# Optimization experiments

Measured on AMD Instinct MI355X. Metric: run time of the kernel, lower is better.

The kernel has to match this reference:

```python
import jax, jax.numpy as jnp
import numpy as np

L, D, H, HD, FF, V, NH, S = 5, 1024, 8, 128, 4096, 2048, 15, 2
EPS = 1e-6
THETA = 10000.0


def rms_norm(x, w):
    x32 = x.astype(jnp.float32)
    y = x32 * jax.lax.rsqrt(jnp.mean(x32 * x32, axis=-1, keepdims=True) + EPS)
    return (y * w.astype(jnp.float32)).astype(x.dtype)


def rotate_half(x):
    x1, x2 = x[..., : HD // 2], x[..., HD // 2:]
    return jnp.concatenate((-x2, x1), axis=-1)


def setup_inputs() -> dict:
    key = jax.random.key(0)
    ks = jax.random.split(key, 20)
    s = 0.02
    inp = {
        "past_hidden": jax.random.normal(ks[0], (1, 1, D), jnp.float32),
        "cb0_token": jax.random.randint(ks[1], (1, 1), 0, V, jnp.int32),
        "codec_emb": jax.random.normal(ks[2], (V, D), jnp.float32) * s,
        "Wq": jax.random.normal(ks[3], (L, D, H * HD), jnp.float32) * s,
        "Wk": jax.random.normal(ks[4], (L, D, H * HD), jnp.float32) * s,
        "Wv": jax.random.normal(ks[5], (L, D, H * HD), jnp.float32) * s,
        "Wo": jax.random.normal(ks[6], (L, H * HD, D), jnp.float32) * s,
        "q_norm_w": jnp.ones((L, HD), jnp.float32),
        "k_norm_w": jnp.ones((L, HD), jnp.float32),
        "ln1_w": jnp.ones((L, D), jnp.float32),
        "ln2_w": jnp.ones((L, D), jnp.float32),
        "Wgate": jax.random.normal(ks[7], (L, D, FF), jnp.float32) * s,
        "Wup": jax.random.normal(ks[8], (L, D, FF), jnp.float32) * s,
        "Wdown": jax.random.normal(ks[9], (L, FF, D), jnp.float32) * s,
        "final_norm_w": jnp.ones((D,), jnp.float32),
        "lm_heads": jax.random.normal(ks[10], (NH, D, V), jnp.float32) * s,
    }
    return inp


def reference(past_hidden, codec_emb, Wq, Wk, Wv, Wo, q_norm_w, k_norm_w,
              ln1_w, ln2_w, Wgate, Wup, Wdown, final_norm_w, lm_heads,
              cb0_token):
    # Embed CB0 token and build 2-token prefill sequence [1, 2, D].
    cb0_embed = codec_emb[cb0_token]            # [1, 1, D]
    h = jnp.concatenate([past_hidden, cb0_embed], axis=1)

    # Rotary cos/sin for positions [0, 1]: [1, 1, S, HD].
    pos = jnp.arange(S, dtype=jnp.float32)
    inv_freq = 1.0 / (THETA ** (jnp.arange(0, HD, 2, dtype=jnp.float32) / HD))
    freqs = pos[:, None] * inv_freq[None, :]    # [S, HD/2]
    emb = jnp.concatenate([freqs, freqs], axis=-1)
    cos = jnp.cos(emb)[None, None]
    sin = jnp.sin(emb)[None, None]

    causal_mask = jnp.array([[0.0, -1e9], [0.0, 0.0]], jnp.float32)
    scale = 1.0 / np.sqrt(HD)

    def layer_step(h, p):
        wq, wk, wv, wo, qn, kn, l1, l2, wg, wu, wd = p
        res = h
        x = rms_norm(h, l1)                     # [1, S, D]
        q = (x @ wq).reshape(1, S, H, HD)
        k = (x @ wk).reshape(1, S, H, HD)
        v = (x @ wv).reshape(1, S, H, HD)
        q = rms_norm(q, qn)                     # per-head qk-norm
        k = rms_norm(k, kn)
        q = q.transpose(0, 2, 1, 3)             # [1, H, S, HD]
        k = k.transpose(0, 2, 1, 3)
        v = v.transpose(0, 2, 1, 3)
        q = q * cos + rotate_half(q) * sin
        k = k * cos + rotate_half(k) * sin
        attn = jnp.einsum('bhqd,bhkd->bhqk', q, k) * scale + causal_mask
        w = jax.nn.softmax(attn.astype(jnp.float32), axis=-1).astype(q.dtype)
        o = jnp.einsum('bhqk,bhkd->bhqd', w, v)
        o = o.transpose(0, 2, 1, 3).reshape(1, S, H * HD) @ wo
        h = res + o
        res = h
        x = rms_norm(h, l2)
        mlp = (jax.nn.silu(x @ wg) * (x @ wu)) @ wd
        return res + mlp, (k, v)

    h, (ks_, vs_) = jax.lax.scan(
        layer_step, h,
        (Wq, Wk, Wv, Wo, q_norm_w, k_norm_w, ln1_w, ln2_w, Wgate, Wup, Wdown))

    h = rms_norm(h, final_norm_w)
    last = h[:, -1, :]                          # [1, D]
    all_logits = jnp.einsum('bd,ndv->nbv', last, lm_heads)  # [15, 1, V]
    # Interleave keys/values per layer: [2L, 1, H, S, HD].
    kv_cache = jnp.stack([ks_, vs_], axis=1).reshape(2 * L, 1, H, S, HD)
    return all_logits, kv_cache
```

## Files before the change

kernel.cpp:

```cpp
#include <hip/hip_runtime.h>
#include <math.h>

#define EPS 1e-6f


__device__ __forceinline__ float red32(float v) {
#pragma unroll
    for (int m = 16; m >= 1; m >>= 1) v += __shfl_xor(v, m, 64);
    return v;
}

__global__ void init_kernel(const float* __restrict__ past_hidden,
                            const float* __restrict__ codec_emb,
                            const int* __restrict__ tok,
                            float* __restrict__ ws,
                            float* __restrict__ logits)
{
    size_t idx = (size_t)blockIdx.x * blockDim.x + threadIdx.x;
    size_t stride = (size_t)gridDim.x * blockDim.x;
    for (size_t i = idx; i < 30720; i += stride) ws[2048 + i] = 0.f;
    for (size_t i = idx; i < 81920; i += stride) ws[43008 + i] = 0.f;
    for (size_t i = idx; i < 30720; i += stride) logits[i] = 0.f;
    int t = tok[0];
    for (size_t i = idx; i < 1024; i += stride) {
        ws[i]        = past_hidden[i];
        ws[1024 + i] = codec_emb[(size_t)t * 1024 + i];
    }
}

template <int S, int R>
__global__ __launch_bounds__(256) void gemv_rms(
    const float* __restrict__ hbuf,
    const float* __restrict__ nw,
    const float* __restrict__ W0,
    const float* __restrict__ W1,
    const float* __restrict__ W2,
    size_t w_zstride,
    float* __restrict__ out,
    int out_sstride, int out_zstride, int N)
{
    __shared__ float xs[S * 1024];
    __shared__ float sstot[S * 4];
    const int t = threadIdx.x;
    const int lane = t & 63;
    const int dp = t >> 6;

    const float* W;
    if (W1) W = (blockIdx.z == 0) ? W0 : ((blockIdx.z == 1) ? W1 : W2);
    else    W = W0 + (size_t)blockIdx.z * w_zstride;
    float* outz = out + (size_t)blockIdx.z * out_zstride;

    const int j = blockIdx.x * 256 + lane * 4;
    const int d0 = blockIdx.y * (4 * R) + dp * R;

    float4 wreg[R];
    const float* Wp = W + (size_t)d0 * N + j;
#pragma unroll
    for (int i = 0; i < R; ++i)
        wreg[i] = *reinterpret_cast<const float4*>(Wp + (size_t)i * N);

    float ss[S];
    {
        float4 nw4 = *reinterpret_cast<const float4*>(nw + t * 4);
#pragma unroll
        for (int s = 0; s < S; ++s) {
            float4 xv = *reinterpret_cast<const float4*>(hbuf + s * 1024 + t * 4);
            ss[s] = xv.x * xv.x + xv.y * xv.y + xv.z * xv.z + xv.w * xv.w;
            float4 xw = make_float4(xv.x * nw4.x, xv.y * nw4.y, xv.z * nw4.z, xv.w * nw4.w);
            *reinterpret_cast<float4*>(&xs[s * 1024 + t * 4]) = xw;
        }
    }
    __syncthreads();

    float acc[S][4];
#pragma unroll
    for (int s = 0; s < S; ++s) { acc[s][0] = acc[s][1] = acc[s][2] = acc[s][3] = 0.f; }
#pragma unroll
    for (int i = 0; i < R; ++i) {
        int dd = d0 + i;
#pragma unroll
        for (int s = 0; s < S; ++s) {
            float xv = xs[s * 1024 + dd];
            acc[s][0] += xv * wreg[i].x; acc[s][1] += xv * wreg[i].y;
            acc[s][2] += xv * wreg[i].z; acc[s][3] += xv * wreg[i].w;
        }
    }

#pragma unroll
    for (int s = 0; s < S; ++s) {
        float v = ss[s];
#pragma unroll
        for (int m = 32; m >= 1; m >>= 1) v += __shfl_xor(v, m, 64);
        if (lane == 0) sstot[s * 4 + dp] = v;
    }
    __syncthreads();
    float sc[S];
#pragma unroll
    for (int s = 0; s < S; ++s) {
        float tot = sstot[s * 4 + 0] + sstot[s * 4 + 1] + sstot[s * 4 + 2] + sstot[s * 4 + 3];
        sc[s] = rsqrtf(tot / 1024.f + EPS);
    }

#pragma unroll
    for (int s = 0; s < S; ++s)
#pragma unroll
        for (int c = 0; c < 4; ++c)
            xs[(dp * S + s) * 256 + lane * 4 + c] = acc[s][c] * sc[s];
    __syncthreads();
    for (int o = t; o < S * 256; o += 256) {
        int s = o >> 8;
        int col = o & 255;
        float sum = 0.f;
#pragma unroll
        for (int p = 0; p < 4; ++p) sum += xs[(p * S + s) * 256 + col];
        atomicAdd(outz + (size_t)s * out_sstride + blockIdx.x * 256 + col, sum);
    }
}

__global__ __launch_bounds__(256) void attn_o_kernel(
    const float* __restrict__ qkv,
    const float* __restrict__ qnw,
    const float* __restrict__ knw,
    const float* __restrict__ W,
    float* __restrict__ out,
    float* __restrict__ kvc)
{
    __shared__ float xs[2048];
    const int t = threadIdx.x;
    const int lane = t & 63;
    const int dp = t >> 6;
    const int j = blockIdx.x * 256 + lane * 4;
    const int d0 = blockIdx.y * 16 + dp * 4;

    float4 wreg[4];
    const float* Wp = W + (size_t)d0 * 1024 + j;
#pragma unroll
    for (int i = 0; i < 4; ++i)
        wreg[i] = *reinterpret_cast<const float4*>(Wp + (size_t)i * 1024);

    const int hh = t >> 5;
    const int g = t & 31;
    float q[2][4], k[2][4], v[2][4];
#pragma unroll
    for (int s = 0; s < 2; ++s)
#pragma unroll
        for (int c = 0; c < 4; ++c) {
            int d = g + c * 32;
            q[s][c] = qkv[s * 3072 +        hh * 128 + d];
            k[s][c] = qkv[s * 3072 + 1024 + hh * 128 + d];
            v[s][c] = qkv[s * 3072 + 2048 + hh * 128 + d];
        }
#pragma unroll
    for (int s = 0; s < 2; ++s) {
        float sq = q[s][0]*q[s][0] + q[s][1]*q[s][1] + q[s][2]*q[s][2] + q[s][3]*q[s][3];
        float sk = k[s][0]*k[s][0] + k[s][1]*k[s][1] + k[s][2]*k[s][2] + k[s][3]*k[s][3];
        sq = red32(sq); sk = red32(sk);
        float qsc = rsqrtf(sq / 128.f + EPS);
        float ksc = rsqrtf(sk / 128.f + EPS);
#pragma unroll
        for (int c = 0; c < 4; ++c) {
            q[s][c] *= qsc * qnw[g + c * 32];
            k[s][c] *= ksc * knw[g + c * 32];
        }
    }
    float inv0 = powf(10000.f, -(float)g / 64.f);
    float inv1 = powf(10000.f, -(float)(g + 32) / 64.f);
    float cA = cosf(inv0), sA = sinf(inv0);
    float cB = cosf(inv1), sB = sinf(inv1);
    float q1[4] = { q[1][0]*cA - q[1][2]*sA, q[1][1]*cB - q[1][3]*sB,
                    q[1][2]*cA + q[1][0]*sA, q[1][3]*cB + q[1][1]*sB };
    float k1[4] = { k[1][0]*cA - k[1][2]*sA, k[1][1]*cB - k[1][3]*sB,
                    k[1][2]*cA + k[1][0]*sA, k[1][3]*cB + k[1][1]*sB };

    if (blockIdx.x == 0 && blockIdx.y == 0) {
#pragma unroll
        for (int c = 0; c < 4; ++c) {
            int d = g + c * 32;
            kvc[hh * 256 +       d] = k[0][c];
            kvc[hh * 256 + 128 + d] = k1[c];
            kvc[2048 + hh * 256 +       d] = v[0][c];
            kvc[2048 + hh * 256 + 128 + d] = v[1][c];
        }
    }

    float p00 = red32(q[0][0]*k[0][0] + q[0][1]*k[0][1] + q[0][2]*k[0][2] + q[0][3]*k[0][3]);
    float p01 = red32(q[0][0]*k1[0]   + q[0][1]*k1[1]   + q[0][2]*k1[2]   + q[0][3]*k1[3]);
    float p10 = red32(q1[0]*k[0][0]   + q1[1]*k[0][1]   + q1[2]*k[0][2]   + q1[3]*k[0][3]);
    float p11 = red32(q1[0]*k1[0]     + q1[1]*k1[1]     + q1[2]*k1[2]     + q1[3]*k1[3]);

    const float scale = 0.08838834764831845f;
    float s00 = p00 * scale, s01 = p01 * scale - 1e9f;
    float m0 = fmaxf(s00, s01);
    float e0 = expf(s00 - m0), e1 = expf(s01 - m0);
    float in0 = 1.f / (e0 + e1);
    float w00 = e0 * in0, w01 = e1 * in0;
    float s10 = p10 * scale, s11 = p11 * scale;
    float m1 = fmaxf(s10, s11);
    float f0 = expf(s10 - m1), f1 = expf(s11 - m1);
    float in1 = 1.f / (f0 + f1);
    float w10 = f0 * in1, w11 = f1 * in1;

#pragma unroll
    for (int c = 0; c < 4; ++c) {
        int d = g + c * 32;
        xs[       hh * 128 + d] = w00 * v[0][c] + w01 * v[1][c];
        xs[1024 + hh * 128 + d] = w10 * v[0][c] + w11 * v[1][c];
    }
    __syncthreads();

    float acc[2][4] = {{0.f,0.f,0.f,0.f},{0.f,0.f,0.f,0.f}};
#pragma unroll
    for (int i = 0; i < 4; ++i) {
        int dd = d0 + i;
#pragma unroll
        for (int s = 0; s < 2; ++s) {
            float xv = xs[s * 1024 + dd];
            acc[s][0] += xv * wreg[i].x; acc[s][1] += xv * wreg[i].y;
            acc[s][2] += xv * wreg[i].z; acc[s][3] += xv * wreg[i].w;
        }
    }
    __syncthreads();
#pragma unroll
    for (int s = 0; s < 2; ++s)
#pragma unroll
        for (int c = 0; c < 4; ++c)
            xs[(dp * 2 + s) * 256 + lane * 4 + c] = acc[s][c];
    __syncthreads();
    for (int o = t; o < 512; o += 256) {
        int s = o >> 8, col = o & 255;
        float sum = 0.f;
#pragma unroll
        for (int p = 0; p < 4; ++p) sum += xs[(p * 2 + s) * 256 + col];
        atomicAdd(out + (size_t)s * 1024 + blockIdx.x * 256 + col, sum);
    }
}

__global__ __launch_bounds__(256) void gemv_down(
    const float* __restrict__ gu,
    const float* __restrict__ W,
    float* __restrict__ out)
{
    __shared__ float a[2][32];
    __shared__ float red[2048];
    const int t = threadIdx.x;
    const int lane = t & 63;
    const int dp = t >> 6;
    const int j = blockIdx.x * 256 + lane * 4;
    const int f0 = blockIdx.y * 32 + dp * 8;

    float4 wreg[8];
    const float* Wp = W + (size_t)f0 * 1024 + j;
#pragma unroll
    for (int i = 0; i < 8; ++i)
        wreg[i] = *reinterpret_cast<const float4*>(Wp + (size_t)i * 1024);

    if (t < 64) {
        int s = t >> 5, x = t & 31;
        int f = blockIdx.y * 32 + x;
        float g = gu[s * 8192 + f];
        float u = gu[s * 8192 + 4096 + f];
        a[s][x] = g / (1.f + expf(-g)) * u;
    }
    __syncthreads();

    float acc[2][4] = {{0.f,0.f,0.f,0.f},{0.f,0.f,0.f,0.f}};
#pragma unroll
    for (int i = 0; i < 8; ++i) {
        int dl = dp * 8 + i;
#pragma unroll
        for (int s = 0; s < 2; ++s) {
            float xv = a[s][dl];
            acc[s][0] += xv * wreg[i].x; acc[s][1] += xv * wreg[i].y;
            acc[s][2] += xv * wreg[i].z; acc[s][3] += xv * wreg[i].w;
        }
    }
#pragma unroll
    for (int s = 0; s < 2; ++s)
#pragma unroll
        for (int c = 0; c < 4; ++c)
            red[(dp * 2 + s) * 256 + lane * 4 + c] = acc[s][c];
    __syncthreads();
    for (int o = t; o < 512; o += 256) {
        int s = o >> 8, col = o & 255;
        float sum = 0.f;
#pragma unroll
        for (int p = 0; p < 4; ++p) sum += red[(p * 2 + s) * 256 + col];
        atomicAdd(out + (size_t)s * 1024 + blockIdx.x * 256 + col, sum);
    }
}

extern "C" void kernel_launch(void* const* d_in, const int* in_sizes, int n_in,
                              void* d_out, int out_size, void* d_ws, size_t ws_size,
                              hipStream_t stream)
{
    const float* past_hidden = (const float*)d_in[0];
    const int*   cb0         = (const int*)d_in[1];
    const float* codec_emb   = (const float*)d_in[2];
    const float* Wq  = (const float*)d_in[3];
    const float* Wk  = (const float*)d_in[4];
    const float* Wv  = (const float*)d_in[5];
    const float* Wo  = (const float*)d_in[6];
    const float* qnw = (const float*)d_in[7];
    const float* knw = (const float*)d_in[8];
    const float* ln1 = (const float*)d_in[9];
    const float* ln2 = (const float*)d_in[10];
    const float* Wg  = (const float*)d_in[11];
    const float* Wu  = (const float*)d_in[12];
    const float* Wd  = (const float*)d_in[13];
    const float* fnw = (const float*)d_in[14];
    const float* lmh = (const float*)d_in[15];

    float* out = (float*)d_out;
    float* ws  = (float*)d_ws;
    float* h      = ws;
    float* qkvb   = ws + 2048;
    float* gub    = ws + 43008;
    float* logits = out;
    float* kvc    = out + 30720;

    init_kernel<<<256, 256, 0, stream>>>(past_hidden, codec_emb, cb0, ws, logits);

    for (int l = 0; l < 5; ++l) {
        const float* wq = Wq + (size_t)l * 1024 * 1024;
        const float* wk = Wk + (size_t)l * 1024 * 1024;
        const float* wv = Wv + (size_t)l * 1024 * 1024;
        const float* wo = Wo + (size_t)l * 1024 * 1024;
        const float* wg = Wg + (size_t)l * 1024 * 4096;
        const float* wu = Wu + (size_t)l * 1024 * 4096;
        const float* wd = Wd + (size_t)l * 4096 * 1024;
        float* qkv = qkvb + (size_t)l * 6144;
        float* gu  = gub  + (size_t)l * 16384;

        gemv_rms<2, 8><<<dim3(4, 32, 3), 256, 0, stream>>>(
            h, ln1 + l * 1024, wq, wk, wv, 0, qkv, 3072, 1024, 1024);
        attn_o_kernel<<<dim3(4, 64), 256, 0, stream>>>(
            qkv, qnw + l * 128, knw + l * 128, wo, h, kvc + (size_t)(2 * l) * 2048);
        gemv_rms<2, 8><<<dim3(16, 32, 2), 256, 0, stream>>>(
            h, ln2 + l * 1024, wg, wu, wu, 0, gu, 8192, 4096, 4096);
        gemv_down<<<dim3(4, 128), 256, 0, stream>>>(gu, wd, h);
    }

    gemv_rms<1, 16><<<dim3(8, 16, 15), 256, 0, stream>>>(
        h + 1024, fnw, lmh, nullptr, nullptr, (size_t)1024 * 2048,
        logits, 2048, 2048, 2048);
}
```

Before: 470.0 us.

## Fuse all layer kernels into one persistent cooperative kernel with grid syncs

Replaces the sequence of about 21 separate kernel launches (init, per-layer QKV, attention+O, gate/up, down, LM head) with a single persistent cooperative kernel that loops over tasks and separates phases with grid.sync(). This removes launch overhead and inter-kernel gaps for a latency-bound decode step. It also retiles the O-projection to 2 rows per warp and the gate/up GEMV to 16 rows per warp. The cost is grid-wide barrier overhead, and the persistent grid size (256–512 blocks) may under-fill the work in some phases.

```diff
diff --git a/kernel.cpp b/kernel.cpp
--- a/kernel.cpp
+++ b/kernel.cpp
@@ -1,5 +1,8 @@
 #include <hip/hip_runtime.h>
+#include <hip/hip_cooperative_groups.h>
 #include <math.h>
+
+namespace cg = cooperative_groups;
 
 #define EPS 1e-6f
 
@@ -10,283 +13,349 @@
     return v;
 }
 
-__global__ void init_kernel(const float* __restrict__ past_hidden,
-                            const float* __restrict__ codec_emb,
-                            const int* __restrict__ tok,
-                            float* __restrict__ ws,
-                            float* __restrict__ logits)
-{
-    size_t idx = (size_t)blockIdx.x * blockDim.x + threadIdx.x;
-    size_t stride = (size_t)gridDim.x * blockDim.x;
-    for (size_t i = idx; i < 30720; i += stride) ws[2048 + i] = 0.f;
-    for (size_t i = idx; i < 81920; i += stride) ws[43008 + i] = 0.f;
-    for (size_t i = idx; i < 30720; i += stride) logits[i] = 0.f;
-    int t = tok[0];
-    for (size_t i = idx; i < 1024; i += stride) {
-        ws[i]        = past_hidden[i];
-        ws[1024 + i] = codec_emb[(size_t)t * 1024 + i];
-    }
-}
-
 template <int S, int R>
-__global__ __launch_bounds__(256) void gemv_rms(
+__device__ __forceinline__ void phase_gemv(
+    float* smem, int t,
     const float* __restrict__ hbuf,
     const float* __restrict__ nw,
-    const float* __restrict__ W0,
-    const float* __restrict__ W1,
-    const float* __restrict__ W2,
-    size_t w_zstride,
-    float* __restrict__ out,
-    int out_sstride, int out_zstride, int N)
+    const float* __restrict__ W0, const float* __restrict__ W1,
+    const float* __restrict__ W2, size_t w_zstride,
+    float* __restrict__ out, int out_sstride, int out_zstride, int N,
+    int nx, int ny, int nz)
 {
-    __shared__ float xs[S * 1024];
-    __shared__ float sstot[S * 4];
-    const int t = threadIdx.x;
+    float* xs = smem;
+    float* sstot = smem + S * 1024;
     const int lane = t & 63;
     const int dp = t >> 6;
-
-    const float* W;
-    if (W1) W = (blockIdx.z == 0) ? W0 : ((blockIdx.z == 1) ? W1 : W2);
-    else    W = W0 + (size_t)blockIdx.z * w_zstride;
-    float* outz = out + (size_t)blockIdx.z * out_zstride;
-
-    const int j = blockIdx.x * 256 + lane * 4;
-    const int d0 = blockIdx.y * (4 * R) + dp * R;
-
-    float4 wreg[R];
-    const float* Wp = W + (size_t)d0 * N + j;
-#pragma unroll
-    for (int i = 0; i < R; ++i)
-        wreg[i] = *reinterpret_cast<const float4*>(Wp + (size_t)i * N);
-
-    float ss[S];
-    {
-        float4 nw4 = *reinterpret_cast<const float4*>(nw + t * 4);
+    const int ntask = nx * ny * nz;
+
+    for (int task = blockIdx.x; task < ntask; task += gridDim.x) {
+        const int z = task / (nx * ny);
+        const int rem = task - z * (nx * ny);
+        const int by = rem / nx;
+        const int bx = rem - by * nx;
+
+        const float* W;
+        if (W1) W = (z == 0) ? W0 : ((z == 1) ? W1 : W2);
+        else    W = W0 + (size_t)z * w_zstride;
+        float* outz = out + (size_t)z * out_zstride;
+
+        const int j = bx * 256 + lane * 4;
+        const int d0 = by * (4 * R) + dp * R;
+
+        float4 wreg[R];
+        const float* Wp = W + (size_t)d0 * N + j;
+#pragma unroll
+        for (int i = 0; i < R; ++i)
+            wreg[i] = *reinterpret_cast<const float4*>(Wp + (size_t)i * N);
+
+        float ss[S];
+        {
+            float4 nw4 = *reinterpret_cast<const float4*>(nw + t * 4);
+#pragma unroll
+            for (int s = 0; s < S; ++s) {
+                float4 xv = *reinterpret_cast<const float4*>(hbuf + s * 1024 + t * 4);
+                ss[s] = xv.x * xv.x + xv.y * xv.y + xv.z * xv.z + xv.w * xv.w;
+                float4 xw = make_float4(xv.x * nw4.x, xv.y * nw4.y, xv.z * nw4.z, xv.w * nw4.w);
+                *reinterpret_cast<float4*>(&xs[s * 1024 + t * 4]) = xw;
+            }
+        }
+        __syncthreads();
+
+        float acc[S][4];
+#pragma unroll
+        for (int s = 0; s < S; ++s) { acc[s][0] = acc[s][1] = acc[s][2] = acc[s][3] = 0.f; }
+#pragma unroll
+        for (int i = 0; i < R; ++i) {
+            int dd = d0 + i;
+#pragma unroll
+            for (int s = 0; s < S; ++s) {
+                float xv = xs[s * 1024 + dd];
+                acc[s][0] += xv * wreg[i].x; acc[s][1] += xv * wreg[i].y;
+                acc[s][2] += xv * wreg[i].z; acc[s][3] += xv * wreg[i].w;
+            }
+        }
+
 #pragma unroll
         for (int s = 0; s < S; ++s) {
-            float4 xv = *reinterpret_cast<const float4*>(hbuf + s * 1024 + t * 4);
-            ss[s] = xv.x * xv.x + xv.y * xv.y + xv.z * xv.z + xv.w * xv.w;
-            float4 xw = make_float4(xv.x * nw4.x, xv.y * nw4.y, xv.z * nw4.z, xv.w * nw4.w);
-            *reinterpret_cast<float4*>(&xs[s * 1024 + t * 4]) = xw;
-        }
-    }
-    __syncthreads();
-
-    float acc[S][4];
-#pragma unroll
-    for (int s = 0; s < S; ++s) { acc[s][0] = acc[s][1] = acc[s][2] = acc[s][3] = 0.f; }
-#pragma unroll
-    for (int i = 0; i < R; ++i) {
-        int dd = d0 + i;
+            float v = ss[s];
+#pragma unroll
+            for (int m = 32; m >= 1; m >>= 1) v += __shfl_xor(v, m, 64);
+            if (lane == 0) sstot[s * 4 + dp] = v;
+        }
+        __syncthreads();
+        float sc[S];
 #pragma unroll
         for (int s = 0; s < S; ++s) {
-            float xv = xs[s * 1024 + dd];
-            acc[s][0] += xv * wreg[i].x; acc[s][1] += xv * wreg[i].y;
-            acc[s][2] += xv * wreg[i].z; acc[s][3] += xv * wreg[i].w;
-        }
-    }
-
-#pragma unroll
-    for (int s = 0; s < S; ++s) {
-        float v = ss[s];
-#pragma unroll
-        for (int m = 32; m >= 1; m >>= 1) v += __shfl_xor(v, m, 64);
-        if (lane == 0) sstot[s * 4 + dp] = v;
-    }
-    __syncthreads();
-    float sc[S];
-#pragma unroll
-    for (int s = 0; s < S; ++s) {
-        float tot = sstot[s * 4 + 0] + sstot[s * 4 + 1] + sstot[s * 4 + 2] + sstot[s * 4 + 3];
-        sc[s] = rsqrtf(tot / 1024.f + EPS);
-    }
-
-#pragma unroll
-    for (int s = 0; s < S; ++s)
-#pragma unroll
-        for (int c = 0; c < 4; ++c)
-            xs[(dp * S + s) * 256 + lane * 4 + c] = acc[s][c] * sc[s];
-    __syncthreads();
-    for (int o = t; o < S * 256; o += 256) {
-        int s = o >> 8;
-        int col = o & 255;
-        float sum = 0.f;
-#pragma unroll
-        for (int p = 0; p < 4; ++p) sum += xs[(p * S + s) * 256 + col];
-        atomicAdd(outz + (size_t)s * out_sstride + blockIdx.x * 256 + col, sum);
-    }
-}
-
-__global__ __launch_bounds__(256) void attn_o_kernel(
+            float tot = sstot[s * 4 + 0] + sstot[s * 4 + 1] + sstot[s * 4 + 2] + sstot[s * 4 + 3];
+            sc[s] = rsqrtf(tot / 1024.f + EPS);
+        }
+
+#pragma unroll
+        for (int s = 0; s < S; ++s)
+#pragma unroll
+            for (int c = 0; c < 4; ++c)
+                xs[(dp * S + s) * 256 + lane * 4 + c] = acc[s][c] * sc[s];
+        __syncthreads();
+        for (int o = t; o < S * 256; o += 256) {
+            int s = o >> 8;
+            int col = o & 255;
+            float sum = 0.f;
+#pragma unroll
+            for (int p = 0; p < 4; ++p) sum += xs[(p * S + s) * 256 + col];
+            atomicAdd(outz + (size_t)s * out_sstride + bx * 256 + col, sum);
+        }
+        __syncthreads();
+    }
+}
+
+__device__ __forceinline__ void phase_attn_o(
+    float* smem, int t,
     const float* __restrict__ qkv,
-    const float* __restrict__ qnw,
-    const float* __restrict__ knw,
+    const float* __restrict__ qnw, const float* __restrict__ knw,
     const float* __restrict__ W,
     float* __restrict__ out,
     float* __restrict__ kvc)
 {
-    __shared__ float xs[2048];
-    const int t = threadIdx.x;
+    float* xs = smem;
     const int lane = t & 63;
     const int dp = t >> 6;
-    const int j = blockIdx.x * 256 + lane * 4;
-    const int d0 = blockIdx.y * 16 + dp * 4;
-
-    float4 wreg[4];
-    const float* Wp = W + (size_t)d0 * 1024 + j;
-#pragma unroll
-    for (int i = 0; i < 4; ++i)
-        wreg[i] = *reinterpret_cast<const float4*>(Wp + (size_t)i * 1024);
-
-    const int hh = t >> 5;
-    const int g = t & 31;
-    float q[2][4], k[2][4], v[2][4];
-#pragma unroll
-    for (int s = 0; s < 2; ++s)
+
+    for (int task = blockIdx.x; task < 512; task += gridDim.x) {
+        const int bx = task & 3;
+        const int by = task >> 2;
+        const int j = bx * 256 + lane * 4;
+        const int d0 = by * 8 + dp * 2;
+
+        float4 wreg[2];
+        const float* Wp = W + (size_t)d0 * 1024 + j;
+#pragma unroll
+        for (int i = 0; i < 2; ++i)
+            wreg[i] = *reinterpret_cast<const float4*>(Wp + (size_t)i * 1024);
+
+        const int hh = t >> 5;
+        const int g = t & 31;
+        float q[2][4], k[2][4], v[2][4];
+#pragma unroll
+        for (int s = 0; s < 2; ++s)
+#pragma unroll
+            for (int c = 0; c < 4; ++c) {
+                int d = g + c * 32;
+                q[s][c] = qkv[s * 3072 +        hh * 128 + d];
+                k[s][c] = qkv[s * 3072 + 1024 + hh * 128 + d];
+                v[s][c] = qkv[s * 3072 + 2048 + hh * 128 + d];
+            }
+#pragma unroll
+        for (int s = 0; s < 2; ++s) {
+            float sq = q[s][0]*q[s][0] + q[s][1]*q[s][1] + q[s][2]*q[s][2] + q[s][3]*q[s][3];
+            float sk = k[s][0]*k[s][0] + k[s][1]*k[s][1] + k[s][2]*k[s][2] + k[s][3]*k[s][3];
+            sq = red32(sq); sk = red32(sk);
+            float qsc = rsqrtf(sq / 128.f + EPS);
+            float ksc = rsqrtf(sk / 128.f + EPS);
+#pragma unroll
+            for (int c = 0; c < 4; ++c) {
+                q[s][c] *= qsc * qnw[g + c * 32];
+                k[s][c] *= ksc * knw[g + c * 32];
+            }
+        }
+        float inv0 = powf(10000.f, -(float)g / 64.f);
+        float inv1 = powf(10000.f, -(float)(g + 32) / 64.f);
+        float cA = cosf(inv0), sA = sinf(inv0);
+        float cB = cosf(inv1), sB = sinf(inv1);
+        float q1[4] = { q[1][0]*cA - q[1][2]*sA, q[1][1]*cB - q[1][3]*sB,
+                        q[1][2]*cA + q[1][0]*sA, q[1][3]*cB + q[1][1]*sB };
+        float k1[4] = { k[1][0]*cA - k[1][2]*sA, k[1][1]*cB - k[1][3]*sB,
+                        k[1][2]*cA + k[1][0]*sA, k[1][3]*cB + k[1][1]*sB };
+
+        if (task == 0) {
+#pragma unroll
+            for (int c = 0; c < 4; ++c) {
+                int d = g + c * 32;
+                kvc[hh * 256 +       d] = k[0][c];
+                kvc[hh * 256 + 128 + d] = k1[c];
+                kvc[2048 + hh * 256 +       d] = v[0][c];
+                kvc[2048 + hh * 256 + 128 + d] = v[1][c];
+            }
+        }
+
+        float p00 = red32(q[0][0]*k[0][0] + q[0][1]*k[0][1] + q[0][2]*k[0][2] + q[0][3]*k[0][3]);
+        float p01 = red32(q[0][0]*k1[0]   + q[0][1]*k1[1]   + q[0][2]*k1[2]   + q[0][3]*k1[3]);
+        float p10 = red32(q1[0]*k[0][0]   + q1[1]*k[0][1]   + q1[2]*k[0][2]   + q1[3]*k[0][3]);
+        float p11 = red32(q1[0]*k1[0]     + q1[1]*k1[1]     + q1[2]*k1[2]     + q1[3]*k1[3]);
+
+        const float scale = 0.08838834764831845f;
+        float s00 = p00 * scale, s01 = p01 * scale - 1e9f;
+        float m0 = fmaxf(s00, s01);
+        float e0 = expf(s00 - m0), e1 = expf(s01 - m0);
+        float in0 = 1.f / (e0 + e1);
+        float w00 = e0 * in0, w01 = e1 * in0;
+        float s10 = p10 * scale, s11 = p11 * scale;
+        float m1 = fmaxf(s10, s11);
+        float f0 = expf(s10 - m1), f1 = expf(s11 - m1);
+        float in1 = 1.f / (f0 + f1);
+        float w10 = f0 * in1, w11 = f1 * in1;
+
 #pragma unroll
         for (int c = 0; c < 4; ++c) {
             int d = g + c * 32;
-            q[s][c] = qkv[s * 3072 +        hh * 128 + d];
-            k[s][c] = qkv[s * 3072 + 1024 + hh * 128 + d];
-            v[s][c] = qkv[s * 3072 + 2048 + hh * 128 + d];
-        }
-#pragma unroll
-    for (int s = 0; s < 2; ++s) {
-        float sq = q[s][0]*q[s][0] + q[s][1]*q[s][1] + q[s][2]*q[s][2] + q[s][3]*q[s][3];
-        float sk = k[s][0]*k[s][0] + k[s][1]*k[s][1] + k[s][2]*k[s][2] + k[s][3]*k[s][3];
-        sq = red32(sq); sk = red32(sk);
-        float qsc = rsqrtf(sq / 128.f + EPS);
-        float ksc = rsqrtf(sk / 128.f + EPS);
-#pragma unroll
-        for (int c = 0; c < 4; ++c) {
-            q[s][c] *= qsc * qnw[g + c * 32];
-            k[s][c] *= ksc * knw[g + c * 32];
-        }
-    }
-    float inv0 = powf(10000.f, -(float)g / 64.f);
-    float inv1 = powf(10000.f, -(float)(g + 32) / 64.f);
-    float cA = cosf(inv0), sA = sinf(inv0);
-    float cB = cosf(inv1), sB = sinf(inv1);
-    float q1[4] = { q[1][0]*cA - q[1][2]*sA, q[1][1]*cB - q[1][3]*sB,
-                    q[1][2]*cA + q[1][0]*sA, q[1][3]*cB + q[1][1]*sB };
-    float k1[4] = { k[1][0]*cA - k[1][2]*sA, k[1][1]*cB - k[1][3]*sB,
-                    k[1][2]*cA + k[1][0]*sA, k[1][3]*cB + k[1][1]*sB };
-
-    if (blockIdx.x == 0 && blockIdx.y == 0) {
-#pragma unroll
-        for (int c = 0; c < 4; ++c) {
-            int d = g + c * 32;
-            kvc[hh * 256 +       d] = k[0][c];
-            kvc[hh * 256 + 128 + d] = k1[c];
-            kvc[2048 + hh * 256 +       d] = v[0][c];
-            kvc[2048 + hh * 256 + 128 + d] = v[1][c];
-        }
-    }
-
-    float p00 = red32(q[0][0]*k[0][0] + q[0][1]*k[0][1] + q[0][2]*k[0][2] + q[0][3]*k[0][3]);
-    float p01 = red32(q[0][0]*k1[0]   + q[0][1]*k1[1]   + q[0][2]*k1[2]   + q[0][3]*k1[3]);
-    float p10 = red32(q1[0]*k[0][0]   + q1[1]*k[0][1]   + q1[2]*k[0][2]   + q1[3]*k[0][3]);
-    float p11 = red32(q1[0]*k1[0]     + q1[1]*k1[1]     + q1[2]*k1[2]     + q1[3]*k1[3]);
-
-    const float scale = 0.08838834764831845f;
-    float s00 = p00 * scale, s01 = p01 * scale - 1e9f;
-    float m0 = fmaxf(s00, s01);
-    float e0 = expf(s00 - m0), e1 = expf(s01 - m0);
-    float in0 = 1.f / (e0 + e1);
-    float w00 = e0 * in0, w01 = e1 * in0;
-    float s10 = p10 * scale, s11 = p11 * scale;
-    float m1 = fmaxf(s10, s11);
-    float f0 = expf(s10 - m1), f1 = expf(s11 - m1);
-    float in1 = 1.f / (f0 + f1);
-    float w10 = f0 * in1, w11 = f1 * in1;
-
-#pragma unroll
-    for (int c = 0; c < 4; ++c) {
-        int d = g + c * 32;
-        xs[       hh * 128 + d] = w00 * v[0][c] + w01 * v[1][c];
-        xs[1024 + hh * 128 + d] = w10 * v[0][c] + w11 * v[1][c];
-    }
-    __syncthreads();
-
-    float acc[2][4] = {{0.f,0.f,0.f,0.f},{0.f,0.f,0.f,0.f}};
-#pragma unroll
-    for (int i = 0; i < 4; ++i) {
-        int dd = d0 + i;
-#pragma unroll
-        for (int s = 0; s < 2; ++s) {
-            float xv = xs[s * 1024 + dd];
-            acc[s][0] += xv * wreg[i].x; acc[s][1] += xv * wreg[i].y;
-            acc[s][2] += xv * wreg[i].z; acc[s][3] += xv * wreg[i].w;
-        }
-    }
-    __syncthreads();
-#pragma unroll
-    for (int s = 0; s < 2; ++s)
-#pragma unroll
-        for (int c = 0; c < 4; ++c)
-            xs[(dp * 2 + s) * 256 + lane * 4 + c] = acc[s][c];
-    __syncthreads();
-    for (int o = t; o < 512; o += 256) {
-        int s = o >> 8, col = o & 255;
-        float sum = 0.f;
-#pragma unroll
-        for (int p = 0; p < 4; ++p) sum += xs[(p * 2 + s) * 256 + col];
-        atomicAdd(out + (size_t)s * 1024 + blockIdx.x * 256 + col, sum);
-    }
-}
-
-__global__ __launch_bounds__(256) void gemv_down(
+            xs[       hh * 128 + d] = w00 * v[0][c] + w01 * v[1][c];
+            xs[1024 + hh * 128 + d] = w10 * v[0][c] + w11 * v[1][c];
+        }
+        __syncthreads();
+
+        float acc[2][4] = {{0.f,0.f,0.f,0.f},{0.f,0.f,0.f,0.f}};
+#pragma unroll
+        for (int i = 0; i < 2; ++i) {
+            int dd = d0 + i;
+#pragma unroll
+            for (int s = 0; s < 2; ++s) {
+                float xv = xs[s * 1024 + dd];
+                acc[s][0] += xv * wreg[i].x; acc[s][1] += xv * wreg[i].y;
+                acc[s][2] += xv * wreg[i].z; acc[s][3] += xv * wreg[i].w;
+            }
+        }
+        __syncthreads();
+#pragma unroll
+        for (int s = 0; s < 2; ++s)
+#pragma unroll
+            for (int c = 0; c < 4; ++c)
+                xs[(dp * 2 + s) * 256 + lane * 4 + c] = acc[s][c];
+        __syncthreads();
+        for (int o = t; o < 512; o += 256) {
+            int s = o >> 8, col = o & 255;
+            float sum = 0.f;
+#pragma unroll
+            for (int p = 0; p < 4; ++p) sum += xs[(p * 2 + s) * 256 + col];
+            atomicAdd(out + (size_t)s * 1024 + bx * 256 + col, sum);
+        }
+        __syncthreads();
+    }
+}
+
+__device__ __forceinline__ void phase_down(
+    float* smem, int t,
     const float* __restrict__ gu,
     const float* __restrict__ W,
     float* __restrict__ out)
 {
-    __shared__ float a[2][32];
-    __shared__ float red[2048];
-    const int t = threadIdx.x;
+    float* red = smem;
+    float* a   = smem + 2048;
     const int lane = t & 63;
     const int dp = t >> 6;
-    const int j = blockIdx.x * 256 + lane * 4;
-    const int f0 = blockIdx.y * 32 + dp * 8;
-
-    float4 wreg[8];
-    const float* Wp = W + (size_t)f0 * 1024 + j;
-#pragma unroll
-    for (int i = 0; i < 8; ++i)
-        wreg[i] = *reinterpret_cast<const float4*>(Wp + (size_t)i * 1024);
-
-    if (t < 64) {
-        int s = t >> 5, x = t & 31;
-        int f = blockIdx.y * 32 + x;
-        float g = gu[s * 8192 + f];
-        float u = gu[s * 8192 + 4096 + f];
-        a[s][x] = g / (1.f + expf(-g)) * u;
-    }
-    __syncthreads();
-
-    float acc[2][4] = {{0.f,0.f,0.f,0.f},{0.f,0.f,0.f,0.f}};
-#pragma unroll
-    for (int i = 0; i < 8; ++i) {
-        int dl = dp * 8 + i;
-#pragma unroll
-        for (int s = 0; s < 2; ++s) {
-            float xv = a[s][dl];
-            acc[s][0] += xv * wreg[i].x; acc[s][1] += xv * wreg[i].y;
-            acc[s][2] += xv * wreg[i].z; acc[s][3] += xv * wreg[i].w;
-        }
-    }
-#pragma unroll
-    for (int s = 0; s < 2; ++s)
-#pragma unroll
-        for (int c = 0; c < 4; ++c)
-            red[(dp * 2 + s) * 256 + lane * 4 + c] = acc[s][c];
-    __syncthreads();
-    for (int o = t; o < 512; o += 256) {
-        int s = o >> 8, col = o & 255;
-        float sum = 0.f;
-#pragma unroll
-        for (int p = 0; p < 4; ++p) sum += red[(p * 2 + s) * 256 + col];
-        atomicAdd(out + (size_t)s * 1024 + blockIdx.x * 256 + col, sum);
-    }
+
+    for (int task = blockIdx.x; task < 512; task += gridDim.x) {
+        const int bx = task & 3;
+        const int by = task >> 2;
+        const int j = bx * 256 + lane * 4;
+        const int f0 = by * 32 + dp * 8;
+
+        float4 wreg[8];
+        const float* Wp = W + (size_t)f0 * 1024 + j;
+#pragma unroll
+        for (int i = 0; i < 8; ++i)
+            wreg[i] = *reinterpret_cast<const float4*>(Wp + (size_t)i * 1024);
+
+        if (t < 64) {
+            int s = t >> 5, x = t & 31;
+            int f = by * 32 + x;
+            float g = gu[s * 8192 + f];
+            float u = gu[s * 8192 + 4096 + f];
+            a[s * 32 + x] = g / (1.f + expf(-g)) * u;
+        }
+        __syncthreads();
+
+        float acc[2][4] = {{0.f,0.f,0.f,0.f},{0.f,0.f,0.f,0.f}};
+#pragma unroll
+        for (int i = 0; i < 8; ++i) {
+            int dl = dp * 8 + i;
+#pragma unroll
+            for (int s = 0; s < 2; ++s) {
+                float xv = a[s * 32 + dl];
+                acc[s][0] += xv * wreg[i].x; acc[s][1] += xv * wreg[i].y;
+                acc[s][2] += xv * wreg[i].z; acc[s][3] += xv * wreg[i].w;
+            }
+        }
+        __syncthreads();
+#pragma unroll
+        for (int s = 0; s < 2; ++s)
+#pragma unroll
+            for (int c = 0; c < 4; ++c)
+                red[(dp * 2 + s) * 256 + lane * 4 + c] = acc[s][c];
+        __syncthreads();
+        for (int o = t; o < 512; o += 256) {
+            int s = o >> 8, col = o & 255;
+            float sum = 0.f;
+#pragma unroll
+            for (int p = 0; p < 4; ++p) sum += red[(p * 2 + s) * 256 + col];
+            atomicAdd(out + (size_t)s * 1024 + bx * 256 + col, sum);
+        }
+        __syncthreads();
+    }
+}
+
+__global__ __launch_bounds__(256, 2) void net_kernel(
+    const float* __restrict__ past_hidden,
+    const int*   __restrict__ tok,
+    const float* __restrict__ codec_emb,
+    const float* __restrict__ Wq, const float* __restrict__ Wk,
+    const float* __restrict__ Wv, const float* __restrict__ Wo,
+    const float* __restrict__ qnw, const float* __restrict__ knw,
+    const float* __restrict__ ln1, const float* __restrict__ ln2,
+    const float* __restrict__ Wg, const float* __restrict__ Wu,
+    const float* __restrict__ Wd, const float* __restrict__ fnw,
+    const float* __restrict__ lmh,
+    float* __restrict__ ws, float* __restrict__ logits, float* __restrict__ kvc)
+{
+    cg::grid_group grid = cg::this_grid();
+    __shared__ float smem[2112];
+    const int t = threadIdx.x;
+    float* h    = ws;
+    float* qkvb = ws + 2048;
+    float* gub  = ws + 43008;
+
+    {
+        const int gt = blockIdx.x * 256 + t;
+        const int gs = gridDim.x * 256;
+        for (int i = gt; i < 30720; i += gs) qkvb[i] = 0.f;
+        for (int i = gt; i < 81920; i += gs) gub[i]  = 0.f;
+        for (int i = gt; i < 30720; i += gs) logits[i] = 0.f;
+        if (blockIdx.x == 0) {
+            int tk = tok[0];
+            for (int i = t; i < 1024; i += 256) {
+                h[i]        = past_hidden[i];
+                h[1024 + i] = codec_emb[(size_t)tk * 1024 + i];
+            }
+        }
+    }
+    grid.sync();
+
+    for (int l = 0; l < 5; ++l) {
+        const float* wq = Wq + (size_t)l * 1024 * 1024;
+        const float* wk = Wk + (size_t)l * 1024 * 1024;
+        const float* wv = Wv + (size_t)l * 1024 * 1024;
+        const float* wo = Wo + (size_t)l * 1024 * 1024;
+        const float* wg = Wg + (size_t)l * 1024 * 4096;
+        const float* wu = Wu + (size_t)l * 1024 * 4096;
+        const float* wd = Wd + (size_t)l * 4096 * 1024;
+        float* qkv = qkvb + l * 6144;
+        float* gu  = gub  + l * 16384;
+
+        phase_gemv<2, 8>(smem, t, h, ln1 + l * 1024, wq, wk, wv, 0,
+                         qkv, 3072, 1024, 1024, 4, 32, 3);
+        grid.sync();
+        phase_attn_o(smem, t, qkv, qnw + l * 128, knw + l * 128, wo, h,
+                     kvc + (size_t)(2 * l) * 2048);
+        grid.sync();
+        phase_gemv<2, 16>(smem, t, h, ln2 + l * 1024, wg, wu, wu, 0,
+                          gu, 8192, 4096, 4096, 16, 16, 2);
+        grid.sync();
+        phase_down(smem, t, gu, wd, h);
+        grid.sync();
+    }
+
+    phase_gemv<1, 16>(smem, t, h + 1024, fnw, lmh, nullptr, nullptr,
+                      (size_t)1024 * 2048, logits, 2048, 2048, 2048,
+                      8, 16, 15);
 }
 
 extern "C" void kernel_launch(void* const* d_in, const int* in_sizes, int n_in,
@@ -310,37 +379,27 @@
     const float* fnw = (const float*)d_in[14];
     const float* lmh = (const float*)d_in[15];
 
-    float* out = (float*)d_out;
-    float* ws  = (float*)d_ws;
-    float* h      = ws;
-    float* qkvb   = ws + 2048;
-    float* gub    = ws + 43008;
-    float* logits = out;
-    float* kvc    = out + 30720;
-
-    init_kernel<<<256, 256, 0, stream>>>(past_hidden, codec_emb, cb0, ws, logits);
-
-    for (int l = 0; l < 5; ++l) {
-        const float* wq = Wq + (size_t)l * 1024 * 1024;
-        const float* wk = Wk + (size_t)l * 1024 * 1024;
-        const float* wv = Wv + (size_t)l * 1024 * 1024;
-        const float* wo = Wo + (size_t)l * 1024 * 1024;
-        const float* wg = Wg + (size_t)l * 1024 * 4096;
-        const float* wu = Wu + (size_t)l * 1024 * 4096;
-        const float* wd = Wd + (size_t)l * 4096 * 1024;
-        float* qkv = qkvb + (size_t)l * 6144;
-        float* gu  = gub  + (size_t)l * 16384;
-
-        gemv_rms<2, 8><<<dim3(4, 32, 3), 256, 0, stream>>>(
-            h, ln1 + l * 1024, wq, wk, wv, 0, qkv, 3072, 1024, 1024);
-        attn_o_kernel<<<dim3(4, 64), 256, 0, stream>>>(
-            qkv, qnw + l * 128, knw + l * 128, wo, h, kvc + (size_t)(2 * l) * 2048);
-        gemv_rms<2, 8><<<dim3(16, 32, 2), 256, 0, stream>>>(
-            h, ln2 + l * 1024, wg, wu, wu, 0, gu, 8192, 4096, 4096);
-        gemv_down<<<dim3(4, 128), 256, 0, stream>>>(gu, wd, h);
-    }
-
-    gemv_rms<1, 16><<<dim3(8, 16, 15), 256, 0, stream>>>(
-        h + 1024, fnw, lmh, nullptr, nullptr, (size_t)1024 * 2048,
-        logits, 2048, 2048, 2048);
-}
+    float* ws     = (float*)d_ws;
+    float* logits = (float*)d_out;
+    float* kvc    = (float*)d_out + 30720;
+
+    static int nblk = 0;
+    if (nblk == 0) {
+        int perCU = 0;
+        if (hipOccupancyMaxActiveBlocksPerMultiprocessor(&perCU, net_kernel, 256, 0) != hipSuccess
+            || perCU < 1) perCU = 1;
+        nblk = perCU * 256;
+        if (nblk > 512) nblk = 512;
+        if (nblk < 256) nblk = 256;
+    }
+
+    void* args[] = {
+        (void*)&past_hidden, (void*)&cb0, (void*)&codec_emb,
+        (void*)&Wq, (void*)&Wk, (void*)&Wv, (void*)&Wo,
+        (void*)&qnw, (void*)&knw, (void*)&ln1, (void*)&ln2,
+        (void*)&Wg, (void*)&Wu, (void*)&Wd, (void*)&fnw, (void*)&lmh,
+        (void*)&ws, (void*)&logits, (void*)&kvc
+    };
+    hipLaunchCooperativeKernel((void*)net_kernel, dim3(nblk), dim3(256),
+                               args, 0, stream);
+}
```

After: 1.059 ms. +125.4%, slower.
